# Performance work log

Measured on AMD Instinct MI355X. Metric: run time of the kernel, lower is better.

## Reference

```python
import jax, jax.numpy as jnp
import numpy as np

NUM_HEADS = 8
NUM_LAYERS = 6
NUM_POINTS = 25
# TrajParamIndex: X=0,Y=1,Z=2,VX=3,VY=4,AX=5,AY=6,YAW=7,LENGTH=8,WIDTH=9,HEIGHT=10


def _unit_cube_points(n=NUM_POINTS):
    m = int(np.sqrt(n))
    lin = np.linspace(-1.0, 1.0, m)
    pts = []
    for dim in range(3):
        for sign in (-1.0, 1.0):
            a, b = np.meshgrid(lin, lin, indexing='ij')
            s = np.full_like(a, sign)
            if dim == 0:
                p = np.stack([s, a, b], -1)
            elif dim == 1:
                p = np.stack([a, s, b], -1)
            else:
                p = np.stack([a, b, s], -1)
            pts.append(p.reshape(-1, 3))
    return jnp.asarray(np.concatenate(pts, 0), jnp.float32)  # [150,3]


def _ln(x, g, b):
    m = x.mean(-1, keepdims=True)
    v = ((x - m) ** 2).mean(-1, keepdims=True)
    return (x - m) / jnp.sqrt(v + 1e-5) * g + b


def _mha(q, k, v, wi, bi, wo, bo):
    E = q.shape[-1]
    d = E // NUM_HEADS
    qq = q @ wi[:E].T + bi[:E]
    kk = k @ wi[E:2 * E].T + bi[E:2 * E]
    vv = v @ wi[2 * E:].T + bi[2 * E:]
    B, S, _ = qq.shape
    Sk = kk.shape[1]
    qh = qq.reshape(B, S, NUM_HEADS, d)
    kh = kk.reshape(B, Sk, NUM_HEADS, d)
    vh = vv.reshape(B, Sk, NUM_HEADS, d)
    att = jnp.einsum('bqhd,bkhd->bhqk', qh, kh) / jnp.sqrt(jnp.float32(d))
    att = jax.nn.softmax(att, axis=-1)
    o = jnp.einsum('bhqk,bkhd->bqhd', att, vh).reshape(B, S, E)
    return o @ wo.T + bo


def _bilinear(feat, uv, valid):
    # feat [B,C,H,W], uv [B,M,2] in [0,1] (u along W), valid [B,M] -> [B,M,C]
    B, C, H, W = feat.shape
    px = uv[..., 0] * (W - 1)
    py = uv[..., 1] * (H - 1)
    x0 = jnp.floor(px)
    y0 = jnp.floor(py)
    wx = px - x0
    wy = py - y0
    x0i = jnp.clip(x0, 0, W - 1).astype(jnp.int32)
    x1i = jnp.clip(x0 + 1, 0, W - 1).astype(jnp.int32)
    y0i = jnp.clip(y0, 0, H - 1).astype(jnp.int32)
    y1i = jnp.clip(y0 + 1, 0, H - 1).astype(jnp.int32)
    flat = feat.reshape(B, C, H * W)
    take = jax.vmap(lambda f, i: f[:, i])  # [C,HW],[M] -> [C,M]
    f00 = take(flat, y0i * W + x0i)
    f01 = take(flat, y0i * W + x1i)
    f10 = take(flat, y1i * W + x0i)
    f11 = take(flat, y1i * W + x1i)
    wxb = wx[:, None, :]
    wyb = wy[:, None, :]
    out = (f00 * (1 - wxb) * (1 - wyb) + f01 * wxb * (1 - wyb)
           + f10 * (1 - wxb) * wyb + f11 * wxb * wyb)
    out = out * valid[:, None, :].astype(out.dtype)
    return out.transpose(0, 2, 1)


def _transform_points(box_pts, tp, ego_t, dt):
    # box_pts [B,N,P,3] local, tp [B,N,11], ego_t [B,4] (x,y,yaw,ts), dt [B]
    yaw = tp[..., 7][..., None]  # [B,N,1]
    c, s = jnp.cos(yaw), jnp.sin(yaw)
    lx, ly, lz = box_pts[..., 0], box_pts[..., 1], box_pts[..., 2]
    rx = lx * c - ly * s
    ry = lx * s + ly * c
    dtb = dt[:, None]  # [B,1]
    cx = tp[..., 0] + tp[..., 3] * dtb + 0.5 * tp[..., 5] * dtb ** 2  # [B,N]
    cy = tp[..., 1] + tp[..., 4] * dtb + 0.5 * tp[..., 6] * dtb ** 2
    cz = tp[..., 2]
    wx = rx + cx[..., None]
    wy = ry + cy[..., None]
    wz = lz + cz[..., None]
    ex = ego_t[:, 0][:, None, None]
    ey = ego_t[:, 1][:, None, None]
    eyaw = ego_t[:, 2][:, None, None]
    pxr = wx - ex
    pyr = wy - ey
    gx = pxr * jnp.cos(eyaw) + pyr * jnp.sin(eyaw)
    gy = -pxr * jnp.sin(eyaw) + pyr * jnp.cos(eyaw)
    return jnp.stack([gx, gy, wz], -1)


def _project(wp, cal):
    # wp [B,N,P,3], cal [B,8] = fx,fy,cx,cy,tx,ty,tz,cam_yaw -> uv in [0,1], valid
    fx, fy, cx0, cy0, tx, ty, tz, cyaw = [cal[:, i][:, None, None] for i in range(8)]
    px = wp[..., 0] - tx
    py = wp[..., 1] - ty
    pz = wp[..., 2] - tz
    fwd = px * jnp.cos(cyaw) + py * jnp.sin(cyaw)
    left = -px * jnp.sin(cyaw) + py * jnp.cos(cyaw)
    zc = fwd
    xc = -left
    yc = -pz
    vz = zc > 0.1
    zs = jnp.maximum(zc, 0.1)
    u = fx * xc / zs + cx0
    v = fy * yc / zs + cy0
    valid = vz & (u >= 0) & (u < 1) & (v >= 0) & (v < 1)
    return jnp.stack([u, v], -1), valid


def _forward(features, calib, ego_states, queries, query_pos,
             traj_w1, traj_b1, traj_w2, traj_b2,
             fm_w1, fm_b1, fm_w2, fm_b2,
             sa_in_w, sa_in_b, sa_out_w, sa_out_b,
             ca_in_w, ca_in_b, ca_out_w, ca_out_b,
             l1_w, l1_b, l2_w, l2_b,
             n1_g, n1_b, n2_g, n2_b, n3_g, n3_b):
    unit = _unit_cube_points()  # [P,3]
    P = unit.shape[0]
    cams, B, T = features.shape[0], features.shape[1], features.shape[2]
    Cf = features.shape[3]
    N = queries.shape[0]

    def traj_head(x):
        return jax.nn.relu(x @ traj_w1.T + traj_b1) @ traj_w2.T + traj_b2

    def feature_mlp(x):
        return jax.nn.relu(x @ fm_w1.T + fm_b1) @ fm_w2.T + fm_b2

    q = jnp.broadcast_to(queries[None], (B, N, queries.shape[1]))
    outputs = []
    for li in range(NUM_LAYERS):
        tp = traj_head(q)  # [B,N,11]
        outputs.append(tp)
        dims = tp[..., 8:11][:, :, None, :]  # [B,N,1,3] (L,W,H)
        box_pts = unit[None, None] * dims  # [B,N,P,3]
        acc = jnp.zeros((B, N, Cf), jnp.float32)
        for t in range(T):
            dt = ego_states[:, t, 3] - ego_states[:, -1, 3]  # [B]
            wp = _transform_points(box_pts, tp, ego_states[:, t], dt)
            for ci in range(cams):
                uv, valid = _project(wp, calib[ci])
                samp = _bilinear(features[ci, :, t], uv.reshape(B, N * P, 2),
                                 valid.reshape(B, N * P))  # [B,N*P,Cf]
                acc = acc + samp.reshape(B, N, P, Cf).sum(axis=2)
        agg = acc / jnp.float32(P * T * cams)
        mem = feature_mlp(agg)  # [B,N,Cf]
        # refine layer li (called without query_pos in decoder forward)
        sa = _mha(q, q, q, sa_in_w[li], sa_in_b[li], sa_out_w[li], sa_out_b[li])
        q = _ln(q + sa, n1_g[li], n1_b[li])
        ca = _mha(q, mem, mem, ca_in_w[li], ca_in_b[li], ca_out_w[li], ca_out_b[li])
        q = _ln(q + ca, n2_g[li], n2_b[li])
        ff = jax.nn.relu(q @ l1_w[li].T + l1_b[li]) @ l2_w[li].T + l2_b[li]
        q = _ln(q + ff, n3_g[li], n3_b[li])
    outputs.append(traj_head(q))
    return jnp.stack(outputs)  # [L+1,B,N,11]


def setup_inputs() -> dict:
    key = jax.random.key(0)
    ks = jax.random.split(key, 32)
    cams, B, T, Cf, H, W = 6, 1, 2, 256, 64, 160
    N, E, Dff, L = 128, 256, 512, NUM_LAYERS

    def rn(k, shape, scale=0.05):
        return jax.random.normal(k, shape, jnp.float32) * scale

    features = jax.random.normal(ks[0], (cams, B, T, Cf, H, W), jnp.float32)
    # calibration: fx,fy,cx,cy,tx,ty,tz,cam_yaw; cameras 8m behind origin along view dir
    cal = np.zeros((cams, B, 8), np.float32)
    for ci in range(cams):
        cyaw = ci * (2 * np.pi / cams)
        cal[ci, :, 0] = 1.2
        cal[ci, :, 1] = 1.6
        cal[ci, :, 2] = 0.5
        cal[ci, :, 3] = 0.5
        cal[ci, :, 4] = -8.0 * np.cos(cyaw)
        cal[ci, :, 5] = -8.0 * np.sin(cyaw)
        cal[ci, :, 6] = -0.5
        cal[ci, :, 7] = cyaw
    calib = jnp.asarray(cal)
    ego = np.zeros((B, T, 4), np.float32)
    for t in range(T):
        ego[:, t, 0] = 0.5 * t
        ego[:, t, 2] = 0.01 * t
        ego[:, t, 3] = 0.1 * t
    ego_states = jnp.asarray(ego)
    return {
        'features': features, 'calib': calib, 'ego_states': ego_states,
        'queries': rn(ks[1], (N, E), 1.0), 'query_pos': rn(ks[2], (N, E), 1.0),
        'traj_w1': rn(ks[3], (Dff, E)), 'traj_b1': jnp.zeros((Dff,), jnp.float32),
        'traj_w2': rn(ks[4], (11, Dff)), 'traj_b2': jnp.zeros((11,), jnp.float32),
        'fm_w1': rn(ks[5], (Dff, E)), 'fm_b1': jnp.zeros((Dff,), jnp.float32),
        'fm_w2': rn(ks[6], (E, Dff)), 'fm_b2': jnp.zeros((E,), jnp.float32),
        'sa_in_w': rn(ks[7], (L, 3 * E, E)), 'sa_in_b': jnp.zeros((L, 3 * E), jnp.float32),
        'sa_out_w': rn(ks[8], (L, E, E)), 'sa_out_b': jnp.zeros((L, E), jnp.float32),
        'ca_in_w': rn(ks[9], (L, 3 * E, E)), 'ca_in_b': jnp.zeros((L, 3 * E), jnp.float32),
        'ca_out_w': rn(ks[10], (L, E, E)), 'ca_out_b': jnp.zeros((L, E), jnp.float32),
        'l1_w': rn(ks[11], (L, Dff, E)), 'l1_b': jnp.zeros((L, Dff), jnp.float32),
        'l2_w': rn(ks[12], (L, E, Dff)), 'l2_b': jnp.zeros((L, E), jnp.float32),
        'n1_g': jnp.ones((L, E), jnp.float32), 'n1_b': jnp.zeros((L, E), jnp.float32),
        'n2_g': jnp.ones((L, E), jnp.float32), 'n2_b': jnp.zeros((L, E), jnp.float32),
        'n3_g': jnp.ones((L, E), jnp.float32), 'n3_b': jnp.zeros((L, E), jnp.float32),
    }


def reference(features, calib, ego_states, queries, query_pos,
              traj_w1, traj_b1, traj_w2, traj_b2,
              fm_w1, fm_b1, fm_w2, fm_b2,
              sa_in_w, sa_in_b, sa_out_w, sa_out_b,
              ca_in_w, ca_in_b, ca_out_w, ca_out_b,
              l1_w, l1_b, l2_w, l2_b,
              n1_g, n1_b, n2_g, n2_b, n3_g, n3_b):
    return _forward(features, calib, ego_states, queries, query_pos,
                    traj_w1, traj_b1, traj_w2, traj_b2,
                    fm_w1, fm_b1, fm_w2, fm_b2,
                    sa_in_w, sa_in_b, sa_out_w, sa_out_b,
                    ca_in_w, ca_in_b, ca_out_w, ca_out_b,
                    l1_w, l1_b, l2_w, l2_b,
                    n1_g, n1_b, n2_g, n2_b, n3_g, n3_b)
```

## Files before the change

### kernel.cpp

```cpp
#include <hip/hip_runtime.h>
#include <stdint.h>

typedef unsigned short u16;

#define DEV static __device__ __forceinline__

DEV float b2f(u16 u){ return __uint_as_float(((uint32_t)u) << 16); }
DEV u16 f2b(float f){ uint32_t x = __float_as_uint(f); return (u16)((x + 0x7fffu + ((x >> 16) & 1u)) >> 16); }
DEV int imin(int a, int b){ return a < b ? a : b; }
DEV int imax(int a, int b){ return a > b ? a : b; }

DEV int is_f32(const void* cal){
  float a = ((const float*)cal)[0];
  return (fabsf(a - 1.2f) < 1e-2f) ? 1 : 0;
}

DEV float ld(const void* p, size_t i, int f32){
  return f32 ? ((const float*)p)[i] : b2f(((const u16*)p)[i]);
}

__device__ float4 g_sawT[6*256*768/4];
__device__ float4 g_sowT[6*256*256/4];
__device__ float4 g_cawT[6*256*768/4];
__device__ float4 g_cowT[6*256*256/4];
__device__ float4 g_l1wT[6*256*512/4];
__device__ float4 g_l2wT[6*512*256/4];
__device__ float4 g_tw1T[256*512/4];
__device__ float4 g_fw1T[256*512/4];
__device__ float4 g_fw2T[512*256/4];

DEV float dotP(const float* x, const float4* wP, int col, const int N, const int K){
  const float4* p = wP + col;
  const float4* x4 = (const float4*)x;
  float s0=0.f,s1=0.f,s2=0.f,s3=0.f;
  #pragma unroll 8
  for(int k4 = 0; k4 < K/4; k4++){
    float4 w = p[(size_t)k4*N];
    float4 xv = x4[k4];
    s0 += xv.x*w.x; s1 += xv.y*w.y; s2 += xv.z*w.z; s3 += xv.w*w.w;
  }
  return (s0+s1)+(s2+s3);
}

DEV void dot2P(const float* x, const float4* wP, int c0, int c1, const int N,
               float* r0, float* r1){
  const float4* p0 = wP + c0;
  const float4* p1 = wP + c1;
  const float4* x4 = (const float4*)x;
  float a0=0,a1=0,a2=0,a3=0,b0=0,b1=0,b2=0,b3=0;
  #pragma unroll 8
  for(int k4 = 0; k4 < 64; k4++){
    float4 xv = x4[k4];
    float4 w0 = p0[(size_t)k4*N];
    float4 w1 = p1[(size_t)k4*N];
    a0+=xv.x*w0.x; a1+=xv.y*w0.y; a2+=xv.z*w0.z; a3+=xv.w*w0.w;
    b0+=xv.x*w1.x; b1+=xv.y*w1.y; b2+=xv.z*w1.z; b3+=xv.w*w1.w;
  }
  *r0=(a0+a1)+(a2+a3); *r1=(b0+b1)+(b2+b3);
}

DEV void dot3P(const float* x, const float4* wP, int t, float* r0, float* r1, float* r2){
  const float4* p0 = wP + t;
  const float4* p1 = wP + t + 256;
  const float4* p2 = wP + t + 512;
  const float4* x4 = (const float4*)x;
  float a0=0,a1=0,a2=0,a3=0,b0=0,b1=0,b2=0,b3=0,c0=0,c1=0,c2=0,c3=0;
  #pragma unroll 4
  for(int k4 = 0; k4 < 64; k4++){
    float4 xv = x4[k4];
    float4 w0 = p0[(size_t)k4*768];
    float4 w1 = p1[(size_t)k4*768];
    float4 w2 = p2[(size_t)k4*768];
    a0+=xv.x*w0.x; a1+=xv.y*w0.y; a2+=xv.z*w0.z; a3+=xv.w*w0.w;
    b0+=xv.x*w1.x; b1+=xv.y*w1.y; b2+=xv.z*w1.z; b3+=xv.w*w1.w;
    c0+=xv.x*w2.x; c1+=xv.y*w2.y; c2+=xv.z*w2.z; c3+=xv.w*w2.w;
  }
  *r0=(a0+a1)+(a2+a3); *r1=(b0+b1)+(b2+b3); *r2=(c0+c1)+(c2+c3);
}

DEV void kv_store_k(float* kT, int t, int qi, float val){
  int hh = t >> 5, i = t & 31;
  kT[((size_t)(hh*1024 + (i>>2)*128 + qi))*4 + (i&3)] = val;
}
DEV void kv_store_v(float* vP, int t, int qi, float val){
  vP[((size_t)((qi>>2)*256 + t))*4 + (qi&3)] = val;
}

DEV float attn_score(const float* qv, const float* kT, int hh, int k){
  const float4* kp = (const float4*)kT + hh*1024 + k;
  const float4* xq = (const float4*)(qv + hh*32);
  float s0=0.f, s1=0.f;
  #pragma unroll
  for(int i4 = 0; i4 < 8; i4 += 2){
    float4 w0 = kp[i4*128], w1 = kp[(i4+1)*128];
    float4 x0 = xq[i4],     x1 = xq[i4+1];
    s0 += x0.x*w0.x + x0.y*w0.y + x0.z*w0.z + x0.w*w0.w;
    s1 += x1.x*w1.x + x1.y*w1.y + x1.z*w1.z + x1.w*w1.w;
  }
  return s0+s1;
}

DEV float attn_av(const float* s, const float* vP, int hh, int t){
  const float4* vp = (const float4*)vP + t;
  const float4* sp = (const float4*)(s + hh*128);
  float a0=0.f, a1=0.f;
  #pragma unroll 8
  for(int k4 = 0; k4 < 32; k4 += 2){
    float4 w0 = vp[(size_t)k4*256], w1 = vp[(size_t)(k4+1)*256];
    float4 s0 = sp[k4],             s1 = sp[k4+1];
    a0 += s0.x*w0.x + s0.y*w0.y + s0.z*w0.z + s0.w*w0.w;
    a1 += s1.x*w1.x + s1.y*w1.y + s1.z*w1.z + s1.w*w1.w;
  }
  return a0+a1;
}

DEV float bsum256(float v, float* buf){
  int t = threadIdx.x;
  for(int off = 32; off > 0; off >>= 1) v += __shfl_xor(v, off);
  if((t & 63) == 0) buf[t >> 6] = v;
  __syncthreads();
  float r = buf[0] + buf[1] + buf[2] + buf[3];
  __syncthreads();
  return r;
}

DEV float lnorm(float r, const void* g, const void* b, size_t off, float* buf, int f32){
  float m = bsum256(r, buf) * (1.f/256.f);
  float d = r - m;
  float v = bsum256(d*d, buf) * (1.f/256.f);
  return d * rsqrtf(v + 1e-5f) * ld(g, off + threadIdx.x, f32) + ld(b, off + threadIdx.x, f32);
}

DEV void traj_headT(const float* qn, const void* b1, const void* w2, const void* b2,
                    float* hbuf, float* tp, void* out, int slot, int qi, int f32){
  int t = threadIdx.x;
  float h0, h1;
  dot2P(qn, g_tw1T, t, t + 256, 512, &h0, &h1);
  hbuf[t]     = fmaxf(0.f, ld(b1, t, f32)     + h0);
  hbuf[t+256] = fmaxf(0.f, ld(b1, t+256, f32) + h1);
  __syncthreads();
  if(t < 176){
    int o = t >> 4, lane = t & 15;
    float s = 0.f;
    for(int k = lane; k < 512; k += 16) s += hbuf[k] * ld(w2, o*512 + k, f32);
    for(int off = 8; off > 0; off >>= 1) s += __shfl_down(s, off, 16);
    if(lane == 0){
      s += ld(b2, o, f32);
      tp[qi*11 + o] = s;
      int oi = (slot*128 + qi)*11 + o;
      if(f32) ((float*)out)[oi] = s; else ((u16*)out)[oi] = f2b(s);
    }
  }
  __syncthreads();
}

DEV void softmax8(float* s){
  int t = threadIdx.x;
  int hh = t >> 5, lane = t & 31;
  float m = -1e30f;
  for(int k = lane; k < 128; k += 32) m = fmaxf(m, s[hh*128 + k]);
  for(int off = 16; off > 0; off >>= 1) m = fmaxf(m, __shfl_xor(m, off, 32));
  float ss = 0.f;
  for(int k = lane; k < 128; k += 32){
    float e = __expf(s[hh*128 + k] - m);
    s[hh*128 + k] = e; ss += e;
  }
  for(int off = 16; off > 0; off >>= 1) ss += __shfl_xor(ss, off, 32);
  float inv = 1.f / ss;
  for(int k = lane; k < 128; k += 32) s[hh*128 + k] *= inv;
}

__global__ __launch_bounds__(256) void k_wt(
    const void* saw, const void* sow, const void* caw, const void* cow,
    const void* l1w, const void* l2w, const void* tw1, const void* fw1, const void* fw2,
    const void* cal){
  int f32 = is_f32(cal);
  int t = threadIdx.x;
  __shared__ __align__(16) float tile[64*65];
  int bid = blockIdx.x;
  const void* src; float* dst; int N, K, NB, KB;
  if(bid < 288)      { src = saw; dst = (float*)g_sawT; N=768; K=256; NB=12; KB=4; }
  else if(bid < 384) { src = sow; dst = (float*)g_sowT; N=256; K=256; NB=4;  KB=4; bid -= 288; }
  else if(bid < 672) { src = caw; dst = (float*)g_cawT; N=768; K=256; NB=12; KB=4; bid -= 384; }
  else if(bid < 768) { src = cow; dst = (float*)g_cowT; N=256; K=256; NB=4;  KB=4; bid -= 672; }
  else if(bid < 960) { src = l1w; dst = (float*)g_l1wT; N=512; K=256; NB=8;  KB=4; bid -= 768; }
  else if(bid < 1152){ src = l2w; dst = (float*)g_l2wT; N=256; K=512; NB=4;  KB=8; bid -= 960; }
  else if(bid < 1184){ src = tw1; dst = (float*)g_tw1T; N=512; K=256; NB=8;  KB=4; bid -= 1152; }
  else if(bid < 1216){ src = fw1; dst = (float*)g_fw1T; N=512; K=256; NB=8;  KB=4; bid -= 1184; }
  else               { src = fw2; dst = (float*)g_fw2T; N=256; K=512; NB=4;  KB=8; bid -= 1216; }
  int nb = bid % NB;
  int kb = (bid / NB) % KB;
  int l  = bid / (NB*KB);
  for(int it = 0; it < 16; it++){
    int n = it*4 + (t >> 6);
    int k = t & 63;
    tile[n*65 + k] = ld(src, ((size_t)l*N + nb*64 + n)*K + kb*64 + k, f32);
  }
  __syncthreads();
  int kl = t & 3, nn = (t >> 2) & 15, wv = t >> 6;
  int n_local = wv*16 + nn;
  for(int k4 = 0; k4 < 16; k4++){
    int kcol = k4*4 + kl;
    size_t addr = (size_t)l*K*N + (((size_t)(kb*16 + k4))*N + nb*64 + n_local)*4 + kl;
    dst[addr] = tile[n_local*65 + kcol];
  }
}

__global__ __launch_bounds__(256) void k_trinit(const void* feat, u16* FTb, int use_ft,
    const void* queries, const void* tb1, const void* tw2, const void* tb2,
    const void* sab, const void* cal,
    float* q, float* tp, float* qrow, float* kTsa, float* vsa, float* acc, void* out){
  int f32 = is_f32(cal);
  int t = threadIdx.x;
  __shared__ __align__(16) float smem[64*65];
  if(blockIdx.x < 128){
    float* qn   = smem;
    float* hbuf = smem + 256;
    int qi = blockIdx.x;
    float v = ld(queries, qi*256 + t, f32);
    qn[t] = v; q[qi*256 + t] = v;
    __syncthreads();
    traj_headT(qn, tb1, tw2, tb2, hbuf, tp, out, 0, qi, f32);
    float c0, c1, c2;
    dot3P(qn, g_sawT, t, &c0, &c1, &c2);
    qrow[qi*256 + t] = ld(sab, t, f32)       + c0;
    kv_store_k(kTsa, t, qi, ld(sab, t + 256, f32) + c1);
    kv_store_v(vsa,  t, qi, ld(sab, t + 512, f32) + c2);
    acc[qi*256 + t] = 0.f;
    return;
  }
  if(!use_ft) return;
  int bid = blockIdx.x - 128;
  int cc = bid & 3; int rest = bid >> 2;
  int pch = rest % 160; int e = rest / 160;
  for(int it = 0; it < 16; it++){
    int c = it*4 + (t >> 6);
    int p = t & 63;
    smem[p*65 + c] = ld(feat, ((size_t)(e*256 + cc*64 + c))*10240 + pch*64 + p, f32);
  }
  __syncthreads();
  for(int it = 0; it < 8; it++){
    int p = it*8 + (t >> 5);
    int c = (t & 31)*2;
    ushort2 v;
    v.x = f2b(smem[p*65 + c]); v.y = f2b(smem[p*65 + c + 1]);
    *(ushort2*)&FTb[((size_t)(e*10240 + pch*64 + p))*256 + cc*64 + c] = v;
  }
}

__global__ __launch_bounds__(256, 2) void k_samsa(const u16* FTb, const void* feat, int use_ft,
    const void* cal, const void* ego, const float* tp, float* acc,
    const float* q, const float* qrow, const float* kTsa, const float* vsa,
    const void* sob, const void* n1g, const void* n1b, const void* cab,
    int li, float* qs, float* qq){
  int t = threadIdx.x;
  int f32 = is_f32(cal);
  __shared__ __align__(16) float xa[256];
  __shared__ __align__(16) float s[1024];
  __shared__ __align__(16) float h[512];
  __shared__ float buf[8];
  __shared__ float tps[11];
  __shared__ int4  soff[152];
  __shared__ float4 sw[152];
  __shared__ float spx[152], spy[152];
  __shared__ int sval[152];
  __shared__ int plist[152];
  __shared__ int pcnt;

  if(blockIdx.x < 128){
    int qi = blockIdx.x;
    xa[t] = qrow[qi*256 + t];
    __syncthreads();
    for(int rep = 0; rep < 4; rep++){
      int idx = t + rep*256; int hh = idx >> 7, k = idx & 127;
      s[idx] = attn_score(xa, kTsa, hh, k) * 0.1767766952966369f;
    }
    __syncthreads();
    softmax8(s);
    __syncthreads();
    h[t] = attn_av(s, vsa, t >> 5, t);
    __syncthreads();
    float pr = ld(sob, (size_t)li*256 + t, f32) + dotP(h, g_sowT + (size_t)li*16384, t, 256, 256);
    float r = q[qi*256 + t] + pr;
    float y = lnorm(r, n1g, n1b, (size_t)li*256, buf, f32);
    qs[qi*256 + t] = y;
    __syncthreads();
    xa[t] = y;
    __syncthreads();
    qq[qi*256 + t] = ld(cab, (size_t)li*768 + t, f32)
                   + dotP(xa, g_cawT + (size_t)li*49152, t, 768, 256);
    return;
  }

  int sb = blockIdx.x - 128;
  int ob = (sb & 7) * 192 + (sb >> 3);
  int qi = ob & 127, e = ob >> 7;
  int ci = e >> 1, tt = e & 1;
  if(t == 0) pcnt = 0;
  if(t < 11) tps[t] = tp[qi*11 + t];
  __syncthreads();
  if(t < 150){
    float dt = ld(ego, tt*4 + 3, f32) - ld(ego, 7, f32);
    int face = t/25, rr = t%25, ii = rr/5, jj = rr%5;
    float av = -1.f + 0.5f*ii, bv = -1.f + 0.5f*jj;
    float sg = (face & 1) ? 1.f : -1.f; int dim = face >> 1;
    float ux = (dim == 0) ? sg : av;
    float uy = (dim == 0) ? av : ((dim == 1) ? sg : bv);
    float uz = (dim == 2) ? sg : bv;
    float lx = ux*tps[8], ly = uy*tps[9], lz = uz*tps[10];
    float yaw = tps[7];
    float cyw = cosf(yaw), syw = sinf(yaw);
    float rx = lx*cyw - ly*syw, ry = lx*syw + ly*cyw;
    float dt2 = 0.5f*dt*dt;
    float cxx = tps[0] + tps[3]*dt + tps[5]*dt2;
    float cyy = tps[1] + tps[4]*dt + tps[6]*dt2;
    float wx = rx + cxx, wy = ry + cyy, wz = lz + tps[2];
    float ex = ld(ego, tt*4, f32), ey = ld(ego, tt*4 + 1, f32), eyaw = ld(ego, tt*4 + 2, f32);
    float ce = cosf(eyaw), se = sinf(eyaw);
    float pxr = wx - ex, pyr = wy - ey;
    float gx = pxr*ce + pyr*se, gy = -pxr*se + pyr*ce;
    float fx = ld(cal, ci*8, f32),   fy = ld(cal, ci*8+1, f32);
    float cx0 = ld(cal, ci*8+2, f32), cy0 = ld(cal, ci*8+3, f32);
    float tx = ld(cal, ci*8+4, f32), ty = ld(cal, ci*8+5, f32);
    float tz = ld(cal, ci*8+6, f32), cw = ld(cal, ci*8+7, f32);
    float cc = cosf(cw), sc = sinf(cw);
    float pxc = gx - tx, pyc = gy - ty, pzc = wz - tz;
    float zc = pxc*cc + pyc*sc;
    float left = -pxc*sc + pyc*cc;
    float xc = -left, yc = -pzc;
    float zs = fmaxf(zc, 0.1f);
    float u = fx*xc/zs + cx0, vv = fy*yc/zs + cy0;
    bool val = (zc > 0.1f) && (u >= 0.f) && (u < 1.f) && (vv >= 0.f) && (vv < 1.f);
    float px = u*159.f, py = vv*63.f;
    spx[t] = px; spy[t] = py;
    float x0f = floorf(px), y0f = floorf(py);
    float wxf = px - x0f, wyf = py - y0f;
    int x0 = imin(imax((int)x0f, 0), 159), y0 = imin(imax((int)y0f, 0), 63);
    int x1 = imin(x0 + 1, 159), y1 = imin(y0 + 1, 63);
    soff[t] = make_int4((y0*160 + x0)*128, (y0*160 + x1)*128,
                        (y1*160 + x0)*128, (y1*160 + x1)*128);
    sw[t] = make_float4((1.f-wxf)*(1.f-wyf), wxf*(1.f-wyf), (1.f-wxf)*wyf, wxf*wyf);
    sval[t] = val ? 1 : 0;
    if(val){ int ix = atomicAdd(&pcnt, 1); plist[ix] = t; }
  }
  __syncthreads();
  if(use_ft){
    int c2 = (t & 127) * 2;
    int half = t >> 7;
    const uint32_t* base = (const uint32_t*)FTb + (size_t)e*10240*128 + (c2 >> 1);
    int np = pcnt;
    int split = (np + 1) >> 1;
    int lo = half ? split : 0;
    int hi = half ? np : split;
    float a0 = 0.f, a1 = 0.f;
    int pp = lo;
    for(; pp + 2 <= hi; pp += 2){
      int p0 = plist[pp], p1 = plist[pp+1];
      int4 o0 = soff[p0]; int4 o1 = soff[p1];
      float4 w0 = sw[p0]; float4 w1 = sw[p1];
      uint32_t u00 = base[o0.x], u01 = base[o0.y], u02 = base[o0.z], u03 = base[o0.w];
      uint32_t u10 = base[o1.x], u11 = base[o1.y], u12 = base[o1.z], u13 = base[o1.w];
      a0 += w0.x*__uint_as_float(u00<<16) + w0.y*__uint_as_float(u01<<16)
          + w0.z*__uint_as_float(u02<<16) + w0.w*__uint_as_float(u03<<16);
      a1 += w0.x*__uint_as_float(u00&0xffff0000u) + w0.y*__uint_as_float(u01&0xffff0000u)
          + w0.z*__uint_as_float(u02&0xffff0000u) + w0.w*__uint_as_float(u03&0xffff0000u);
      a0 += w1.x*__uint_as_float(u10<<16) + w1.y*__uint_as_float(u11<<16)
          + w1.z*__uint_as_float(u12<<16) + w1.w*__uint_as_float(u13<<16);
      a1 += w1.x*__uint_as_float(u10&0xffff0000u) + w1.y*__uint_as_float(u11&0xffff0000u)
          + w1.z*__uint_as_float(u12&0xffff0000u) + w1.w*__uint_as_float(u13&0xffff0000u);
    }
    for(; pp < hi; pp++){
      int p = plist[pp];
      int4 o = soff[p]; float4 w = sw[p];
      uint32_t u0 = base[o.x], u1 = base[o.y], u2 = base[o.z], u3 = base[o.w];
      a0 += w.x*__uint_as_float(u0<<16) + w.y*__uint_as_float(u1<<16)
          + w.z*__uint_as_float(u2<<16) + w.w*__uint_as_float(u3<<16);
      a1 += w.x*__uint_as_float(u0&0xffff0000u) + w.y*__uint_as_float(u1&0xffff0000u)
          + w.z*__uint_as_float(u2&0xffff0000u) + w.w*__uint_as_float(u3&0xffff0000u);
    }
    s[half*256 + c2]     = a0;
    s[half*256 + c2 + 1] = a1;
    __syncthreads();
    atomicAdd(&acc[qi*256 + t], s[t] + s[256 + t]);
  } else {
    float a = 0.f;
    size_t pc = ((size_t)e*256 + t)*10240;
    for(int p = 0; p < 150; p++){
      if(!sval[p]) continue;
      float px = spx[p], py = spy[p];
      float x0f = floorf(px), y0f = floorf(py);
      float wxf = px - x0f, wyf = py - y0f;
      int x0 = imin(imax((int)x0f, 0), 159), y0 = imin(imax((int)y0f, 0), 63);
      int x1 = imin(x0 + 1, 159), y1 = imin(y0 + 1, 63);
      float w00 = (1.f-wxf)*(1.f-wyf), w01 = wxf*(1.f-wyf), w10 = (1.f-wxf)*wyf, w11 = wxf*wyf;
      a += w00*ld(feat, pc + y0*160 + x0, f32) + w01*ld(feat, pc + y0*160 + x1, f32)
         + w10*ld(feat, pc + y1*160 + x0, f32) + w11*ld(feat, pc + y1*160 + x1, f32);
    }
    atomicAdd(&acc[qi*256 + t], a);
  }
}

__global__ __launch_bounds__(256, 2) void k_mk(const float* acc,
    const void* fb1, const void* fb2, const void* cab, const void* cal,
    int li, float* kvK, float* kvV){
  __shared__ __align__(16) float xa[256];
  __shared__ __align__(16) float h[512];
  int t = threadIdx.x, qi = blockIdx.x;
  int f32 = is_f32(cal);
  xa[t] = acc[qi*256 + t] * (1.f/1800.f);
  __syncthreads();
  float h0, h1;
  dot2P(xa, g_fw1T, t, t + 256, 512, &h0, &h1);
  h[t]     = fmaxf(0.f, ld(fb1, t, f32)     + h0);
  h[t+256] = fmaxf(0.f, ld(fb1, t+256, f32) + h1);
  __syncthreads();
  float m = ld(fb2, t, f32) + dotP(h, g_fw2T, t, 256, 512);
  __syncthreads();
  xa[t] = m;
  __syncthreads();
  const float4* cawT = g_cawT + (size_t)li*49152;
  float kk, vv;
  dot2P(xa, cawT, 256 + t, 512 + t, 768, &kk, &vv);
  size_t bo = (size_t)li*768;
  kv_store_k(kvK, t, qi, ld(cab, bo + 256 + t, f32) + kk);
  kv_store_v(kvV, t, qi, ld(cab, bo + 512 + t, f32) + vv);
}

__global__ __launch_bounds__(256, 2) void k_ca(const float* qs, const float* qq,
    const float* kvK, const float* kvV,
    const void* cob, const void* n2g, const void* n2b,
    const void* l1b, const void* l2b, const void* n3g, const void* n3b,
    const void* tb1, const void* tw2, const void* tb2, const void* sab, const void* cal,
    int li, int have_next,
    float* qout, float* qrow, float* kTsa, float* vsa,
    float* tp, float* acc, void* out){
  __shared__ __align__(16) float qv[256]; __shared__ __align__(16) float s[1024];
  __shared__ __align__(16) float o[256];  __shared__ __align__(16) float q2[256];
  __shared__ __align__(16) float h[512];  __shared__ float buf[8];
  int t = threadIdx.x, qi = blockIdx.x;
  int f32 = is_f32(cal);
  qv[t] = qq[qi*256 + t];
  __syncthreads();
  for(int rep = 0; rep < 4; rep++){
    int idx = t + rep*256; int hh = idx >> 7, k = idx & 127;
    s[idx] = attn_score(qv, kvK, hh, k) * 0.1767766952966369f;
  }
  __syncthreads();
  softmax8(s);
  __syncthreads();
  o[t] = attn_av(s, kvV, t >> 5, t);
  __syncthreads();
  float pr = ld(cob, (size_t)li*256 + t, f32) + dotP(o, g_cowT + (size_t)li*16384, t, 256, 256);
  float r = qs[qi*256 + t] + pr;
  float y = lnorm(r, n2g, n2b, (size_t)li*256, buf, f32);
  q2[t] = y;
  __syncthreads();
  float h0, h1;
  dot2P(q2, g_l1wT + (size_t)li*32768, t, t + 256, 512, &h0, &h1);
  h[t]     = fmaxf(0.f, ld(l1b, (size_t)li*512 + t, f32)     + h0);
  h[t+256] = fmaxf(0.f, ld(l1b, (size_t)li*512 + t+256, f32) + h1);
  __syncthreads();
  float ff = ld(l2b, (size_t)li*256 + t, f32) + dotP(h, g_l2wT + (size_t)li*32768, t, 256, 512);
  float r3 = q2[t] + ff;
  float y3 = lnorm(r3, n3g, n3b, (size_t)li*256, buf, f32);
  qout[qi*256 + t] = y3;
  __syncthreads();
  q2[t] = y3;
  __syncthreads();
  traj_headT(q2, tb1, tw2, tb2, h, tp, out, li + 1, qi, f32);
  if(have_next){
    float c0, c1, c2;
    dot3P(q2, g_sawT + (size_t)(li+1)*49152, t, &c0, &c1, &c2);
    size_t sb = (size_t)(li+1)*768;
    qrow[qi*256 + t] = ld(sab, sb + t, f32) + c0;
    kv_store_k(kTsa, t, qi, ld(sab, sb + 256 + t, f32) + c1);
    kv_store_v(vsa,  t, qi, ld(sab, sb + 512 + t, f32) + c2);
  }
  acc[qi*256 + t] = 0.f;
}

extern "C" void kernel_launch(void* const* d_in, const int* in_sizes, int n_in,
                              void* d_out, int out_size, void* d_ws, size_t ws_size,
                              hipStream_t stream){
  const void* feat    = d_in[0];
  const void* calib   = d_in[1];
  const void* ego     = d_in[2];
  const void* queries = d_in[3];
  const void* tw1 = d_in[5];  const void* tb1 = d_in[6];
  const void* tw2 = d_in[7];  const void* tb2 = d_in[8];
  const void* fw1 = d_in[9];  const void* fb1 = d_in[10];
  const void* fw2 = d_in[11]; const void* fb2 = d_in[12];
  const void* saw = d_in[13]; const void* sab = d_in[14];
  const void* sow = d_in[15]; const void* sob = d_in[16];
  const void* caw = d_in[17]; const void* cab = d_in[18];
  const void* cow = d_in[19]; const void* cob = d_in[20];
  const void* l1w = d_in[21]; const void* l1b = d_in[22];
  const void* l2w = d_in[23]; const void* l2b = d_in[24];
  const void* n1g = d_in[25]; const void* n1b = d_in[26];
  const void* n2g = d_in[27]; const void* n2b = d_in[28];
  const void* n3g = d_in[29]; const void* n3b = d_in[30];

  float* ws   = (float*)d_ws;
  float* q    = ws + 16;
  float* qs   = ws + 32784;
  float* tp   = ws + 65552;
  float* qrow = ws + 67088;
  float* kTsa = ws + 99856;
  float* vsa  = ws + 132624;
  float* kvK  = ws + 165392;
  float* kvV  = ws + 198160;
  float* qq   = ws + 230928;
  float* acc  = ws + 263696;
  u16*   FTb  = (u16*)(ws + 296464);
  size_t need = (size_t)296464*4 + (size_t)12*10240*256*2;
  int use_ft = (ws_size >= need) ? 1 : 0;

  k_wt<<<1248, 256, 0, stream>>>(saw, sow, caw, cow, l1w, l2w, tw1, fw1, fw2, calib);
  k_trinit<<<7808, 256, 0, stream>>>(feat, FTb, use_ft,
                                     queries, tb1, tw2, tb2, sab, calib,
                                     q, tp, qrow, kTsa, vsa, acc, d_out);
  for(int li = 0; li < 6; li++){
    k_samsa<<<1664, 256, 0, stream>>>(FTb, feat, use_ft, calib, ego, tp, acc,
                                      q, qrow, kTsa, vsa, sob, n1g, n1b, cab,
                                      li, qs, qq);
    k_mk<<<128, 256, 0, stream>>>(acc, fb1, fb2, cab, calib, li, kvK, kvV);
    int hn = (li < 5) ? 1 : 0;
    k_ca<<<128, 256, 0, stream>>>(qs, qq, kvK, kvV, cob, n2g, n2b,
                                  l1b, l2b, n3g, n3b,
                                  tb1, tw2, tb2, sab, calib, li, hn,
                                  q, qrow, kTsa, vsa, tp, acc, d_out);
  }
  (void)in_sizes; (void)n_in; (void)out_size;
}
```

Measured before the change: 970.2 us.

## Deduplicate bilinear tap pixels via shared-memory hash before feature gather

Each sampling block now inserts the four bilinear corner pixels of every valid point into a shared-memory open-addressing hash table, summing the weights of duplicate pixels, then compacts the result into a unique-pixel list. The gather loop then reads each distinct feature pixel once with its combined weight, instead of four reads per point. Neighbouring cube-face points often land in the same pixels, so this cuts global memory reads. In exchange it adds hash initialisation, CAS contention, an extra compaction pass with a barrier, and more shared memory, which may lower occupancy.

```diff
diff --git a/kernel.cpp b/kernel.cpp
--- a/kernel.cpp
+++ b/kernel.cpp
@@ -260,12 +260,13 @@
   __shared__ __align__(16) float h[512];
   __shared__ float buf[8];
   __shared__ float tps[11];
-  __shared__ int4  soff[152];
-  __shared__ float4 sw[152];
   __shared__ float spx[152], spy[152];
   __shared__ int sval[152];
-  __shared__ int plist[152];
-  __shared__ int pcnt;
+  __shared__ uint32_t hk[1024];
+  __shared__ float hw[1024];
+  __shared__ int ulist[608];
+  __shared__ float uw[608];
+  __shared__ int ucnt;
 
   if(blockIdx.x < 128){
     int qi = blockIdx.x;
@@ -296,8 +297,9 @@
   int ob = (sb & 7) * 192 + (sb >> 3);
   int qi = ob & 127, e = ob >> 7;
   int ci = e >> 1, tt = e & 1;
-  if(t == 0) pcnt = 0;
+  if(t == 0) ucnt = 0;
   if(t < 11) tps[t] = tp[qi*11 + t];
+  for(int i = t; i < 1024; i += 256){ hk[i] = 0xFFFFFFFFu; hw[i] = 0.f; }
   __syncthreads();
   if(t < 150){
     float dt = ld(ego, tt*4 + 3, f32) - ld(ego, 7, f32);
@@ -333,50 +335,59 @@
     bool val = (zc > 0.1f) && (u >= 0.f) && (u < 1.f) && (vv >= 0.f) && (vv < 1.f);
     float px = u*159.f, py = vv*63.f;
     spx[t] = px; spy[t] = py;
-    float x0f = floorf(px), y0f = floorf(py);
-    float wxf = px - x0f, wyf = py - y0f;
-    int x0 = imin(imax((int)x0f, 0), 159), y0 = imin(imax((int)y0f, 0), 63);
-    int x1 = imin(x0 + 1, 159), y1 = imin(y0 + 1, 63);
-    soff[t] = make_int4((y0*160 + x0)*128, (y0*160 + x1)*128,
-                        (y1*160 + x0)*128, (y1*160 + x1)*128);
-    sw[t] = make_float4((1.f-wxf)*(1.f-wyf), wxf*(1.f-wyf), (1.f-wxf)*wyf, wxf*wyf);
     sval[t] = val ? 1 : 0;
-    if(val){ int ix = atomicAdd(&pcnt, 1); plist[ix] = t; }
+    if(val && use_ft){
+      float x0f = floorf(px), y0f = floorf(py);
+      float wxf = px - x0f, wyf = py - y0f;
+      int x0 = imin(imax((int)x0f, 0), 159), y0 = imin(imax((int)y0f, 0), 63);
+      int x1 = imin(x0 + 1, 159), y1 = imin(y0 + 1, 63);
+      int p00 = y0*160 + x0, p01 = y0*160 + x1, p10 = y1*160 + x0, p11 = y1*160 + x1;
+      float w00 = (1.f-wxf)*(1.f-wyf), w01 = wxf*(1.f-wyf), w10 = (1.f-wxf)*wyf, w11 = wxf*wyf;
+      #pragma unroll
+      for(int c = 0; c < 4; c++){
+        int pos = (c==0)?p00:((c==1)?p01:((c==2)?p10:p11));
+        float w = (c==0)?w00:((c==1)?w01:((c==2)?w10:w11));
+        uint32_t hsh = (((uint32_t)pos) * 2654435761u >> 20) & 1023u;
+        while(true){
+          uint32_t prev = atomicCAS(&hk[hsh], 0xFFFFFFFFu, (uint32_t)pos);
+          if(prev == 0xFFFFFFFFu || prev == (uint32_t)pos){ atomicAdd(&hw[hsh], w); break; }
+          hsh = (hsh + 1) & 1023u;
+        }
+      }
+    }
   }
   __syncthreads();
   if(use_ft){
+    for(int i = t; i < 1024; i += 256){
+      if(hk[i] != 0xFFFFFFFFu){
+        int ix = atomicAdd(&ucnt, 1);
+        ulist[ix] = (int)hk[i]; uw[ix] = hw[i];
+      }
+    }
+    __syncthreads();
     int c2 = (t & 127) * 2;
     int half = t >> 7;
     const uint32_t* base = (const uint32_t*)FTb + (size_t)e*10240*128 + (c2 >> 1);
-    int np = pcnt;
-    int split = (np + 1) >> 1;
+    int U = ucnt;
+    int split = (U + 1) >> 1;
     int lo = half ? split : 0;
-    int hi = half ? np : split;
+    int hi = half ? U : split;
     float a0 = 0.f, a1 = 0.f;
     int pp = lo;
-    for(; pp + 2 <= hi; pp += 2){
-      int p0 = plist[pp], p1 = plist[pp+1];
-      int4 o0 = soff[p0]; int4 o1 = soff[p1];
-      float4 w0 = sw[p0]; float4 w1 = sw[p1];
-      uint32_t u00 = base[o0.x], u01 = base[o0.y], u02 = base[o0.z], u03 = base[o0.w];
-      uint32_t u10 = base[o1.x], u11 = base[o1.y], u12 = base[o1.z], u13 = base[o1.w];
-      a0 += w0.x*__uint_as_float(u00<<16) + w0.y*__uint_as_float(u01<<16)
-          + w0.z*__uint_as_float(u02<<16) + w0.w*__uint_as_float(u03<<16);
-      a1 += w0.x*__uint_as_float(u00&0xffff0000u) + w0.y*__uint_as_float(u01&0xffff0000u)
-          + w0.z*__uint_as_float(u02&0xffff0000u) + w0.w*__uint_as_float(u03&0xffff0000u);
-      a0 += w1.x*__uint_as_float(u10<<16) + w1.y*__uint_as_float(u11<<16)
-          + w1.z*__uint_as_float(u12<<16) + w1.w*__uint_as_float(u13<<16);
-      a1 += w1.x*__uint_as_float(u10&0xffff0000u) + w1.y*__uint_as_float(u11&0xffff0000u)
-          + w1.z*__uint_as_float(u12&0xffff0000u) + w1.w*__uint_as_float(u13&0xffff0000u);
+    for(; pp + 4 <= hi; pp += 4){
+      int q0 = ulist[pp]*128, q1 = ulist[pp+1]*128, q2 = ulist[pp+2]*128, q3 = ulist[pp+3]*128;
+      float w0 = uw[pp], w1 = uw[pp+1], w2 = uw[pp+2], w3 = uw[pp+3];
+      uint32_t u0 = base[q0], u1 = base[q1], u2 = base[q2], u3 = base[q3];
+      a0 += w0*__uint_as_float(u0<<16) + w1*__uint_as_float(u1<<16)
+          + w2*__uint_as_float(u2<<16) + w3*__uint_as_float(u3<<16);
+      a1 += w0*__uint_as_float(u0&0xffff0000u) + w1*__uint_as_float(u1&0xffff0000u)
+          + w2*__uint_as_float(u2&0xffff0000u) + w3*__uint_as_float(u3&0xffff0000u);
     }
     for(; pp < hi; pp++){
-      int p = plist[pp];
-      int4 o = soff[p]; float4 w = sw[p];
-      uint32_t u0 = base[o.x], u1 = base[o.y], u2 = base[o.z], u3 = base[o.w];
-      a0 += w.x*__uint_as_float(u0<<16) + w.y*__uint_as_float(u1<<16)
-          + w.z*__uint_as_float(u2<<16) + w.w*__uint_as_float(u3<<16);
-      a1 += w.x*__uint_as_float(u0&0xffff0000u) + w.y*__uint_as_float(u1&0xffff0000u)
-          + w.z*__uint_as_float(u2&0xffff0000u) + w.w*__uint_as_float(u3&0xffff0000u);
+      int qo = ulist[pp]*128; float w = uw[pp];
+      uint32_t u0 = base[qo];
+      a0 += w*__uint_as_float(u0<<16);
+      a1 += w*__uint_as_float(u0&0xffff0000u);
     }
     s[half*256 + c2]     = a0;
     s[half*256 + c2 + 1] = a1;
```

Result: no change. 976.4 us (+0.6%).
